# Kernel optimization log

Hardware: AMD Instinct MI355X
Metric: run time of the kernel (lower is better)

Reference implementation:

```python
import jax, jax.numpy as jnp
import numpy as np

B, TX, TS = 64, 2048, 10
D, L, NMELS, MAXR, R = 256, 1024, 80, 20, 2


def gru_cell(x, h, wih, whh, bih, bhh):
    # torch GRUCell: gates ordered (r, z, n)
    gi = x @ wih.T + bih
    gh = h @ whh.T + bhh
    ir, iz, inn = jnp.split(gi, 3, axis=-1)
    hr, hz, hn = jnp.split(gh, 3, axis=-1)
    r = jax.nn.sigmoid(ir + hr)
    z = jax.nn.sigmoid(iz + hz)
    n = jnp.tanh(inn + r * hn)
    return (1.0 - z) * n + z * h


def lstm_cell(x, h, c, wih, whh, bih, bhh):
    # torch LSTMCell: gates ordered (i, f, g, o)
    g = x @ wih.T + bih + h @ whh.T + bhh
    i, f, gg, o = jnp.split(g, 4, axis=-1)
    c_new = jax.nn.sigmoid(f) * c + jax.nn.sigmoid(i) * jnp.tanh(gg)
    h_new = jax.nn.sigmoid(o) * jnp.tanh(c_new)
    return h_new, c_new


def attention(enc, query, W, v):
    # u = v @ tanh(enc + W q); softmax over time
    qp = query @ W.T                                  # [B, D]
    u = jnp.tanh(enc + qp[:, None, :]) @ v            # [B, T]
    scores = jax.nn.softmax(u, axis=-1)               # [B, T]
    ctx = jnp.einsum('bt,btd->bd', scores, enc)       # [B, D]
    return scores, ctx


def setup_inputs() -> dict:
    key = jax.random.key(0)
    ks = jax.random.split(key, 40)
    n = lambda i, shape, s=0.02: jax.random.normal(ks[i], shape, dtype=jnp.float32) * s
    return {
        'encoder_seq': n(0, (B, TX, D), 1.0),
        'style_embed': n(1, (B, TS, D), 1.0),
        'prenet_in': n(2, (B, NMELS), 1.0),
        'h_text': n(3, (B, D), 1.0), 'h_style': n(4, (B, D), 1.0), 'h_attn': n(5, (B, D), 1.0),
        'h_r1': n(6, (B, L), 1.0), 'h_r2': n(7, (B, L), 1.0),
        'c_r1': n(8, (B, L), 1.0), 'c_r2': n(9, (B, L), 1.0),
        'cv_text': n(10, (B, D), 1.0), 'cv_style': n(11, (B, D), 1.0), 'cv': n(12, (B, D), 1.0),
        'fc1_w': n(13, (256, NMELS)), 'fc1_b': jnp.zeros((256,), jnp.float32),
        'fc2_w': n(14, (128, 256)), 'fc2_b': jnp.zeros((128,), jnp.float32),
        'tW': n(15, (D, D)), 'tv': n(16, (D,)),
        'sW': n(17, (D, D)), 'sv': n(18, (D,)),
        't_wih': n(19, (3 * D, D + 128)), 't_whh': n(20, (3 * D, D)),
        't_bih': jnp.zeros((3 * D,), jnp.float32), 't_bhh': jnp.zeros((3 * D,), jnp.float32),
        's_wih': n(21, (3 * D, D + 128)), 's_whh': n(22, (3 * D, D)),
        's_bih': jnp.zeros((3 * D,), jnp.float32), 's_bhh': jnp.zeros((3 * D,), jnp.float32),
        'a_wih': n(23, (3 * D, D + 128)), 'a_whh': n(24, (3 * D, D)),
        'a_bih': jnp.zeros((3 * D,), jnp.float32), 'a_bhh': jnp.zeros((3 * D,), jnp.float32),
        'ri_w': n(25, (L, 2 * D)), 'ri_b': jnp.zeros((L,), jnp.float32),
        'l1_wih': n(26, (4 * L, L)), 'l1_whh': n(27, (4 * L, L)),
        'l1_bih': jnp.zeros((4 * L,), jnp.float32), 'l1_bhh': jnp.zeros((4 * L,), jnp.float32),
        'l2_wih': n(28, (4 * L, L)), 'l2_whh': n(29, (4 * L, L)),
        'l2_bih': jnp.zeros((4 * L,), jnp.float32), 'l2_bhh': jnp.zeros((4 * L,), jnp.float32),
        'mp_w': n(30, (NMELS * MAXR, L)),
        't': 0,
    }


def reference(encoder_seq, style_embed, prenet_in, h_text, h_style, h_attn,
              h_r1, h_r2, c_r1, c_r2, cv_text, cv_style, cv,
              fc1_w, fc1_b, fc2_w, fc2_b, tW, tv, sW, sv,
              t_wih, t_whh, t_bih, t_bhh, s_wih, s_whh, s_bih, s_bhh,
              a_wih, a_whh, a_bih, a_bhh, ri_w, ri_b,
              l1_wih, l1_whh, l1_bih, l1_bhh, l2_wih, l2_whh, l2_bih, l2_bhh,
              mp_w, t):
    # PreNet (eval mode: no dropout)
    p = jax.nn.relu(prenet_in @ fc1_w.T + fc1_b)
    p = jax.nn.relu(p @ fc2_w.T + fc2_b)                      # [B, 128]

    text_in = jnp.concatenate([cv_text, p], axis=-1)          # [B, D+128]
    style_in = jnp.concatenate([cv_style, p], axis=-1)
    attn_in = jnp.concatenate([cv, p], axis=-1)

    h_text = gru_cell(text_in, h_text, t_wih, t_whh, t_bih, t_bhh)
    text_scores, cv_text = attention(encoder_seq, h_text, tW, tv)

    h_style = gru_cell(style_in, h_style, s_wih, s_whh, s_bih, s_bhh)
    style_scores, cv_style = attention(style_embed, h_style, sW, sv)

    cv_new = cv_text                                          # context_vec = text_context_vec
    h_attn = gru_cell(attn_in, h_attn, a_wih, a_whh, a_bih, a_bhh)

    x = jnp.concatenate([cv_new, h_attn], axis=1) @ ri_w.T + ri_b  # [B, L]
    h_r1, c_r1 = lstm_cell(x, h_r1, c_r1, l1_wih, l1_whh, l1_bih, l1_bhh)
    x = x + h_r1
    h_r2, c_r2 = lstm_cell(x, h_r2, c_r2, l2_wih, l2_whh, l2_bih, l2_bhh)
    x = x + h_r2

    mels = (x @ mp_w.T).reshape(B, NMELS, MAXR)[:, :, :R]     # [B, n_mels, r]
    return mels
```

## Files before the change

### kernel.cpp

```cpp
#include <hip/hip_runtime.h>
#include <hip/hip_bf16.h>

typedef unsigned short u16;
typedef unsigned int   u32;
typedef __attribute__((ext_vector_type(8))) short bf16x8;
typedef __attribute__((ext_vector_type(4))) float f32x4;

#define NB   64
#define NTX  2048
#define ND   256
#define NL   1024

#if __has_builtin(__builtin_amdgcn_exp2f)
#define EXP2F(x) __builtin_amdgcn_exp2f(x)
#else
#define EXP2F(x) exp2f(x)
#endif

__device__ __forceinline__ float rcp_fast(float x){
  float r;
  asm volatile("v_rcp_f32 %0, %1" : "=v"(r) : "v"(x));
  return r;
}

__device__ __forceinline__ u16 f2bf(float f){
  union { float f; u32 u; } c; c.f = f;
  return (u16)((c.u + 0x7fffu + ((c.u >> 16) & 1u)) >> 16);
}
__device__ __forceinline__ u32 pk2(float a, float b){
  return (u32)f2bf(a) | ((u32)f2bf(b) << 16);
}
__device__ __forceinline__ float sigmf(float x){ return 1.f/(1.f+__expf(-x)); }
__device__ __forceinline__ float tanhf_fast(float x){
  x = fminf(fmaxf(x, -15.f), 15.f);
  float e = __expf(2.f*x);
  return (e - 1.f) / (e + 1.f);
}
__device__ __forceinline__ float tanh_pade(float x){
  x = fminf(fmaxf(x, -4.f), 4.f);
  float t = x*x;
  float n = ((t + 378.f)*t + 17325.f)*t + 135135.f;
  float d = ((28.f*t + 3150.f)*t + 62370.f)*t + 135135.f;
  return x * n * rcp_fast(d);
}
__device__ __forceinline__ float dot_rowf(const float* __restrict__ row,
                                          const float* __restrict__ x, int K4){
  float acc = 0.f;
  for (int j = 0; j < K4; ++j){
    float4 w = *(const float4*)(row + j*4);
    const float* xp = x + j*4;
    acc += w.x*xp[0] + w.y*xp[1] + w.z*xp[2] + w.w*xp[3];
  }
  return acc;
}

__global__ __launch_bounds__(256) void k_pre1(
    const float* __restrict__ cv_text, const float* __restrict__ cv,
    const float* __restrict__ h_text,  const float* __restrict__ h_attn,
    const float* __restrict__ prenet_in,
    const float* __restrict__ fc1_w, const float* __restrict__ fc1_b,
    const float* __restrict__ h_r1, const float* __restrict__ h_r2,
    float* __restrict__ xtext, float* __restrict__ xattn,
    float* __restrict__ htT,  float* __restrict__ haT,
    float* __restrict__ p1T,
    u16* __restrict__ hb1, u16* __restrict__ hb2)
{
  __shared__ float ld[64][65];
  const int blk = blockIdx.x, tid = threadIdx.x;
  if (blk < 16){
    int a = blk >> 2; int c0 = (blk & 3)*64;
    const float* src = (a==0)?cv_text:(a==1)?cv:(a==2)?h_text:h_attn;
    float* dst = (a==0)?xtext:(a==1)?xattn:(a==2)?htT:haT;
    const int r = tid >> 2, q = tid & 3;
    #pragma unroll
    for (int i = 0; i < 4; ++i){
      float4 v = *(const float4*)(src + (size_t)r*256 + c0 + q*16 + i*4);
      ld[r][q*16+i*4+0] = v.x; ld[r][q*16+i*4+1] = v.y;
      ld[r][q*16+i*4+2] = v.z; ld[r][q*16+i*4+3] = v.w;
    }
    __syncthreads();
    const int cc = tid >> 2;
    #pragma unroll
    for (int i = 0; i < 4; ++i){
      int b0 = q*16 + i*4;
      float4 o = { ld[b0+0][cc], ld[b0+1][cc], ld[b0+2][cc], ld[b0+3][cc] };
      *(float4*)(dst + (size_t)(c0+cc)*64 + b0) = o;
    }
  } else if (blk < 80){
    const int wave = tid >> 6, lane = tid & 63;
    const int n = (blk - 16)*4 + wave;
    float acc = fc1_b[n];
    const float* wr = fc1_w + (size_t)n*80;
    const float* xr = prenet_in + (size_t)lane*80;
    #pragma unroll
    for (int k = 0; k < 80; k += 4){
      float4 w = *(const float4*)(wr + k);
      acc += w.x*xr[k] + w.y*xr[k+1] + w.z*xr[k+2] + w.w*xr[k+3];
    }
    p1T[n*64 + lane] = fmaxf(acc, 0.f);
  } else {
    const int t2 = blk - 80;
    const float* src = (t2 < 32) ? h_r1 : h_r2;
    u16* dst = (t2 < 32) ? hb1 : hb2;
    const int base = (t2 & 31)*2048 + tid*8;
    float4 a = *(const float4*)(src + base);
    float4 b = *(const float4*)(src + base + 4);
    uint4 o = { pk2(a.x,a.y), pk2(a.z,a.w), pk2(b.x,b.y), pk2(b.z,b.w) };
    *(uint4*)(dst + base) = o;
  }
}

__global__ __launch_bounds__(256) void k_pre2(
    const float* __restrict__ p1T,
    const float* __restrict__ fc2_w, const float* __restrict__ fc2_b,
    float* __restrict__ xtext, float* __restrict__ xattn)
{
  const int tid = threadIdx.x, w = tid >> 6, lane = tid & 63;
  const int n = blockIdx.x;
  __shared__ float red[4][64];
  float acc = 0.f;
  const float* wr = fc2_w + (size_t)n*256 + w*64;
  const float* xb = p1T + w*64*64 + lane;
  #pragma unroll
  for (int k = 0; k < 64; k += 4){
    float4 wv = *(const float4*)(wr + k);
    acc += wv.x*xb[(k+0)*64] + wv.y*xb[(k+1)*64]
         + wv.z*xb[(k+2)*64] + wv.w*xb[(k+3)*64];
  }
  red[w][lane] = acc;
  __syncthreads();
  if (w == 0){
    float v = fmaxf(red[0][lane]+red[1][lane]+red[2][lane]+red[3][lane] + fc2_b[n], 0.f);
    xtext[(size_t)(256+n)*64 + lane] = v;
    xattn[(size_t)(256+n)*64 + lane] = v;
  }
}

__global__ __launch_bounds__(512) void k_gru(
    const float* __restrict__ t_wih, const float* __restrict__ t_whh,
    const float* __restrict__ t_bih, const float* __restrict__ t_bhh,
    const float* __restrict__ a_wih, const float* __restrict__ a_whh,
    const float* __restrict__ a_bih, const float* __restrict__ a_bhh,
    const float* __restrict__ xtext, const float* __restrict__ xattn,
    const float* __restrict__ htT,  const float* __restrict__ haT,
    float* __restrict__ htnT, u16* __restrict__ xrib)
{
  const int tid = threadIdx.x, w = tid >> 6, lane = tid & 63;
  const int isA = blockIdx.x >= 256;
  const int d = blockIdx.x & 255;
  const float* wih = isA ? a_wih : t_wih;
  const float* whh = isA ? a_whh : t_whh;
  const float* xT  = isA ? xattn : xtext;
  const float* hT  = isA ? haT   : htT;
  __shared__ float red[8][6][64];
  float s0=0.f,s1=0.f,s2=0.f,s3=0.f,s4=0.f,s5=0.f;
  {
    const float* wr = wih + (size_t)d*384       + w*48;
    const float* wz = wih + (size_t)(256+d)*384 + w*48;
    const float* wn = wih + (size_t)(512+d)*384 + w*48;
    const float* xb = xT + w*48*64 + lane;
    #pragma unroll 4
    for (int k = 0; k < 48; k += 4){
      float4 ar = *(const float4*)(wr + k);
      float4 az = *(const float4*)(wz + k);
      float4 an = *(const float4*)(wn + k);
      float x0 = xb[(k+0)*64], x1 = xb[(k+1)*64];
      float x2 = xb[(k+2)*64], x3 = xb[(k+3)*64];
      s0 += ar.x*x0 + ar.y*x1 + ar.z*x2 + ar.w*x3;
      s1 += az.x*x0 + az.y*x1 + az.z*x2 + az.w*x3;
      s2 += an.x*x0 + an.y*x1 + an.z*x2 + an.w*x3;
    }
  }
  {
    const float* vr = whh + (size_t)d*256       + w*32;
    const float* vz = whh + (size_t)(256+d)*256 + w*32;
    const float* vn = whh + (size_t)(512+d)*256 + w*32;
    const float* hb = hT + w*32*64 + lane;
    #pragma unroll 4
    for (int k = 0; k < 32; k += 4){
      float4 ar = *(const float4*)(vr + k);
      float4 az = *(const float4*)(vz + k);
      float4 an = *(const float4*)(vn + k);
      float h0 = hb[(k+0)*64], h1 = hb[(k+1)*64];
      float h2 = hb[(k+2)*64], h3 = hb[(k+3)*64];
      s3 += ar.x*h0 + ar.y*h1 + ar.z*h2 + ar.w*h3;
      s4 += az.x*h0 + az.y*h1 + az.z*h2 + az.w*h3;
      s5 += an.x*h0 + an.y*h1 + an.z*h2 + an.w*h3;
    }
  }
  red[w][0][lane]=s0; red[w][1][lane]=s1; red[w][2][lane]=s2;
  red[w][3][lane]=s3; red[w][4][lane]=s4; red[w][5][lane]=s5;
  __syncthreads();
  if (w == 0){
    const float* bih = isA ? a_bih : t_bih;
    const float* bhh = isA ? a_bhh : t_bhh;
    float g6[6];
    #pragma unroll
    for (int i = 0; i < 6; ++i){
      float a = 0.f;
      #pragma unroll
      for (int ww = 0; ww < 8; ++ww) a += red[ww][i][lane];
      g6[i] = a;
    }
    float gir = bih[d]     + g6[0];
    float giz = bih[256+d] + g6[1];
    float gin = bih[512+d] + g6[2];
    float ghr = bhh[d]     + g6[3];
    float ghz = bhh[256+d] + g6[4];
    float ghn = bhh[512+d] + g6[5];
    float hd = hT[d*64 + lane];
    float r  = sigmf(gir + ghr), z = sigmf(giz + ghz);
    float nn = tanhf_fast(gin + r*ghn);
    float hnew = (1.f - z)*nn + z*hd;
    if (isA) xrib[(size_t)lane*512 + 256 + d] = f2bf(hnew);
    else     htnT[(size_t)d*64 + lane]        = hnew;
  }
}

__global__ __launch_bounds__(256) void k_qp(
    const float* __restrict__ tWm, const float* __restrict__ htnT,
    float* __restrict__ qp)
{
  const int tid = threadIdx.x, w = tid >> 6, lane = tid & 63;
  const int d = blockIdx.x;
  __shared__ float red[4][64];
  float acc = 0.f;
  const float* wr = tWm + (size_t)d*256 + w*64;
  const float* xb = htnT + w*64*64 + lane;
  #pragma unroll
  for (int k = 0; k < 64; k += 4){
    float4 wv = *(const float4*)(wr + k);
    acc += wv.x*xb[(k+0)*64] + wv.y*xb[(k+1)*64]
         + wv.z*xb[(k+2)*64] + wv.w*xb[(k+3)*64];
  }
  red[w][lane] = acc;
  __syncthreads();
  if (w == 0)
    qp[lane*ND + d] = red[0][lane]+red[1][lane]+red[2][lane]+red[3][lane];
}

__global__ __launch_bounds__(256) void k_attn_part(
    const float* __restrict__ enc, const float* __restrict__ qp,
    const float* __restrict__ tv,  float* __restrict__ attnP)
{
  const int tid = threadIdx.x, b = blockIdx.x, ch = blockIdx.y;
  const int w = tid >> 6, lane = tid & 63;
  const float L2E = 1.4426950408f;
  __shared__ float qpL[256], vL[256];
  __shared__ float part[4][16][65];
  __shared__ float wbc[4][16];
  __shared__ float ctxL[4][256], sL[4];
  qpL[tid] = qp[b*ND + tid];
  vL[tid]  = tv[tid];
  __syncthreads();

  const float q0 = qpL[lane*4+0], q1 = qpL[lane*4+1], q2 = qpL[lane*4+2], q3 = qpL[lane*4+3];
  const float v0 = vL[lane*4+0],  v1 = vL[lane*4+1],  v2 = vL[lane*4+2],  v3 = vL[lane*4+3];

  const float* base = enc + ((size_t)b*NTX + (size_t)ch*64 + w*16)*ND + lane*4;
  float4 ev[16];
  #pragma unroll
  for (int i = 0; i < 16; ++i) ev[i] = *(const float4*)(base + (size_t)i*ND);

  #pragma unroll
  for (int i = 0; i < 16; ++i){
    float t0 = tanh_pade(ev[i].x + q0);
    float t1 = tanh_pade(ev[i].y + q1);
    float t2 = tanh_pade(ev[i].z + q2);
    float t3 = tanh_pade(ev[i].w + q3);
    part[w][i][lane] = v0*t0 + v1*t1 + v2*t2 + v3*t3;
  }
  __syncthreads();

  {
    const int rr = lane >> 2, q4 = lane & 3;
    float s = 0.f;
    #pragma unroll
    for (int i = 0; i < 16; ++i) s += part[w][rr][q4*16 + i];
    s += __shfl_xor(s, 1);
    s += __shfl_xor(s, 2);
    if (q4 == 0) wbc[w][rr] = EXP2F(s * L2E);
  }
  __syncthreads();

  float cx0=0.f, cx1=0.f, cx2=0.f, cx3=0.f, sacc=0.f;
  #pragma unroll
  for (int r = 0; r < 16; ++r){
    float wv = wbc[w][r];
    sacc += wv;
    cx0 = __builtin_fmaf(wv, ev[r].x, cx0);
    cx1 = __builtin_fmaf(wv, ev[r].y, cx1);
    cx2 = __builtin_fmaf(wv, ev[r].z, cx2);
    cx3 = __builtin_fmaf(wv, ev[r].w, cx3);
  }
  ctxL[w][lane*4+0]=cx0; ctxL[w][lane*4+1]=cx1;
  ctxL[w][lane*4+2]=cx2; ctxL[w][lane*4+3]=cx3;
  if (lane == 0) sL[w] = sacc;
  __syncthreads();
  float c = ctxL[0][tid]+ctxL[1][tid]+ctxL[2][tid]+ctxL[3][tid];
  float* dst = attnP + ((size_t)b*32 + ch)*257;
  dst[tid] = c;
  if (tid == 0) dst[256] = sL[0]+sL[1]+sL[2]+sL[3];
}

__global__ __launch_bounds__(256) void k_attn_red(
    const float* __restrict__ attnP, u16* __restrict__ xrib)
{
  const int tid = threadIdx.x, b = blockIdx.x;
  float c = 0.f, s = 0.f;
  for (int ch = 0; ch < 32; ++ch){
    const float* src = attnP + ((size_t)b*32 + ch)*257;
    c += src[tid]; s += src[256];
  }
  xrib[(size_t)b*512 + tid] = f2bf(c / s);
}


__global__ __launch_bounds__(512) void k_mm_ri(
    const u16* __restrict__ xrib, const float* __restrict__ ri_w,
    const float* __restrict__ ri_b, float* __restrict__ x0,
    u16* __restrict__ x0b)
{
  __shared__ float Rs[8][4][4][65];
  const int tid = threadIdx.x, lane = tid & 63, w = tid >> 6;
  const int n0 = blockIdx.x * 16;
  f32x4 acc[4];
  #pragma unroll
  for (int i = 0; i < 4; ++i) acc[i] = (f32x4){0.f,0.f,0.f,0.f};
  const int kbase = w*64;
  const float* wr = ri_w + (size_t)(n0 + (lane & 15))*512 + kbase + (lane >> 4)*8;
  const u16* xs = xrib + (size_t)(lane & 15)*512 + kbase + (lane >> 4)*8;
  #pragma unroll
  for (int t = 0; t < 2; ++t){
    float4 wa = *(const float4*)(wr + t*32);
    float4 wb = *(const float4*)(wr + t*32 + 4);
    union { bf16x8 v; uint4 u; } bf;
    bf.u.x = pk2(wa.x,wa.y); bf.u.y = pk2(wa.z,wa.w);
    bf.u.z = pk2(wb.x,wb.y); bf.u.w = pk2(wb.z,wb.w);
    #pragma unroll
    for (int fb = 0; fb < 4; ++fb){
      union { bf16x8 v; uint4 u; } af;
      af.u = *(const uint4*)(xs + fb*16*512 + t*32);
      acc[fb] = __builtin_amdgcn_mfma_f32_16x16x32_bf16(af.v, bf.v, acc[fb], 0, 0, 0);
    }
  }
  #pragma unroll
  for (int fb = 0; fb < 4; ++fb)
    #pragma unroll
    for (int r = 0; r < 4; ++r) Rs[w][fb][r][lane] = acc[fb][r];
  __syncthreads();
  if (tid < 256){
    const int b = tid >> 2, c4 = (tid & 3)*4;
    const int fb = b >> 4, q = (b >> 2) & 3, reg = b & 3;
    #pragma unroll
    for (int cc = 0; cc < 4; ++cc){
      const int c = c4 + cc;
      float v = ri_b[n0 + c];
      #pragma unroll
      for (int ww = 0; ww < 8; ++ww) v += Rs[ww][fb][reg][q*16 + c];
      x0[(size_t)b*1024 + n0 + c]  = v;
      x0b[(size_t)b*1024 + n0 + c] = f2bf(v);
    }
  }
}

__global__ __launch_bounds__(1024) void k_lstm(
    const float* __restrict__ Wih, const float* __restrict__ Whh,
    const u16* __restrict__ xb, const u16* __restrict__ hb,
    const float* __restrict__ bih, const float* __restrict__ bhh,
    const float* __restrict__ c_in,
    const float* __restrict__ xin, float* __restrict__ xout,
    u16* __restrict__ xoutb)
{
  __shared__ float Rs[16][4][4][65];
  const int tid = threadIdx.x, lane = tid & 63, w = tid >> 6;
  const int j0 = blockIdx.x * 4;
  const float* W = (w < 8) ? Wih : Whh;
  const u16*   X = (w < 8) ? xb  : hb;
  const int kbase = (w & 7) * 128;

  f32x4 acc[4];
  #pragma unroll
  for (int i = 0; i < 4; ++i) acc[i] = (f32x4){0.f,0.f,0.f,0.f};
  const int r16 = lane & 15;
  const int g = r16 >> 2, jq = r16 & 3;
  const float* wr = W + (size_t)(g*1024 + j0 + jq)*1024 + kbase + (lane >> 4)*8;
  #pragma unroll
  for (int t = 0; t < 4; ++t){
    float4 wa = *(const float4*)(wr + t*32);
    float4 wb = *(const float4*)(wr + t*32 + 4);
    union { bf16x8 v; uint4 u; } bf;
    bf.u.x = pk2(wa.x,wa.y); bf.u.y = pk2(wa.z,wa.w);
    bf.u.z = pk2(wb.x,wb.y); bf.u.w = pk2(wb.z,wb.w);
    #pragma unroll
    for (int fb = 0; fb < 4; ++fb){
      union { bf16x8 v; uint4 u; } af;
      af.u = *(const uint4*)(X + (size_t)(fb*16 + r16)*1024 + kbase + (lane >> 4)*8 + t*32);
      acc[fb] = __builtin_amdgcn_mfma_f32_16x16x32_bf16(af.v, bf.v, acc[fb], 0, 0, 0);
    }
  }
  #pragma unroll
  for (int fb = 0; fb < 4; ++fb)
    #pragma unroll
    for (int r = 0; r < 4; ++r) Rs[w][fb][r][lane] = acc[fb][r];
  __syncthreads();

  if (tid < 256){
    const int b  = tid >> 2, jq2 = tid & 3;
    const int j  = j0 + jq2;
    const int fb = b >> 4, q = (b >> 2) & 3, reg = b & 3;
    float gate[4];
    #pragma unroll
    for (int gg = 0; gg < 4; ++gg){
      const int li = q*16 + gg*4 + jq2;
      float a = bih[gg*1024 + j] + bhh[gg*1024 + j];
      #pragma unroll
      for (int ww = 0; ww < 16; ++ww) a += Rs[ww][fb][reg][li];
      gate[gg] = a;
    }
    float ii = sigmf(gate[0]), ff = sigmf(gate[1]);
    float gv = tanhf_fast(gate[2]), oo = sigmf(gate[3]);
    float cc = ff * c_in[(size_t)b*1024 + j] + ii * gv;
    float hh = oo * tanhf_fast(cc);
    float xo = xin[(size_t)b*1024 + j] + hh;
    xout[(size_t)b*1024 + j]  = xo;
    xoutb[(size_t)b*1024 + j] = f2bf(xo);
  }
}

__global__ __launch_bounds__(256) void k_mels(
    const float* __restrict__ x2, const float* __restrict__ mp_w,
    float* __restrict__ out)
{
  const int tid = threadIdx.x, b = blockIdx.x;
  __shared__ float xL[NL];
  #pragma unroll
  for (int i = 0; i < 4; ++i){
    int j = tid + 256*i;
    xL[j] = x2[(size_t)b*NL + j];
  }
  __syncthreads();
  if (tid < 160){
    int m = tid >> 1, r = tid & 1;
    float acc = dot_rowf(mp_w + (size_t)(m*20 + r)*NL, xL, 256);
    out[b*160 + tid] = acc;
  }
}

extern "C" void kernel_launch(void* const* d_in, const int* in_sizes, int n_in,
                              void* d_out, int out_size, void* d_ws, size_t ws_size,
                              hipStream_t stream)
{
  (void)in_sizes; (void)n_in; (void)out_size; (void)ws_size;
  const float* enc     = (const float*)d_in[0];
  const float* pre_in  = (const float*)d_in[2];
  const float* h_text  = (const float*)d_in[3];
  const float* h_attn  = (const float*)d_in[5];
  const float* h_r1    = (const float*)d_in[6];
  const float* h_r2    = (const float*)d_in[7];
  const float* c_r1    = (const float*)d_in[8];
  const float* c_r2    = (const float*)d_in[9];
  const float* cv_text = (const float*)d_in[10];
  const float* cv      = (const float*)d_in[12];
  const float* fc1_w   = (const float*)d_in[13];
  const float* fc1_b   = (const float*)d_in[14];
  const float* fc2_w   = (const float*)d_in[15];
  const float* fc2_b   = (const float*)d_in[16];
  const float* tWm     = (const float*)d_in[17];
  const float* tv      = (const float*)d_in[18];
  const float* t_wih   = (const float*)d_in[21];
  const float* t_whh   = (const float*)d_in[22];
  const float* t_bih   = (const float*)d_in[23];
  const float* t_bhh   = (const float*)d_in[24];
  const float* a_wih   = (const float*)d_in[29];
  const float* a_whh   = (const float*)d_in[30];
  const float* a_bih   = (const float*)d_in[31];
  const float* a_bhh   = (const float*)d_in[32];
  const float* ri_w    = (const float*)d_in[33];
  const float* ri_b    = (const float*)d_in[34];
  const float* l1_wih  = (const float*)d_in[35];
  const float* l1_whh  = (const float*)d_in[36];
  const float* l1_bih  = (const float*)d_in[37];
  const float* l1_bhh  = (const float*)d_in[38];
  const float* l2_wih  = (const float*)d_in[39];
  const float* l2_whh  = (const float*)d_in[40];
  const float* l2_bih  = (const float*)d_in[41];
  const float* l2_bhh  = (const float*)d_in[42];
  const float* mp_w    = (const float*)d_in[43];

  float* ws    = (float*)d_ws;
  float* qp    = ws;
  float* attnP = qp    + 16384;
  float* x0    = attnP + 526336;
  float* x1    = x0    + 65536;
  float* x2    = x1    + 65536;
  float* xtext = x2    + 65536;
  float* xattn = xtext + 24576;
  float* htT   = xattn + 24576;
  float* haT   = htT   + 16384;
  float* htnT  = haT   + 16384;
  float* p1T   = htnT  + 16384;
  u16*   hb1   = (u16*)(p1T + 16384);
  u16*   hb2   = hb1 + 65536;
  u16*   xrib  = hb2 + 65536;
  u16*   x0b   = xrib + 32768;
  u16*   x1b   = x0b + 65536;
  u16*   x2b   = x1b + 65536;

  k_pre1<<<144, 256, 0, stream>>>(cv_text, cv, h_text, h_attn,
      pre_in, fc1_w, fc1_b, h_r1, h_r2,
      xtext, xattn, htT, haT, p1T, hb1, hb2);
  k_pre2<<<128, 256, 0, stream>>>(p1T, fc2_w, fc2_b, xtext, xattn);
  k_gru<<<512, 512, 0, stream>>>(t_wih, t_whh, t_bih, t_bhh,
      a_wih, a_whh, a_bih, a_bhh, xtext, xattn, htT, haT, htnT, xrib);
  k_qp<<<256, 256, 0, stream>>>(tWm, htnT, qp);

  k_attn_part<<<dim3(64,32), 256, 0, stream>>>(enc, qp, tv, attnP);
  k_attn_red<<<64, 256, 0, stream>>>(attnP, xrib);

  k_mm_ri<<<64, 512, 0, stream>>>(xrib, ri_w, ri_b, x0, x0b);

  k_lstm<<<256, 1024, 0, stream>>>(l1_wih, l1_whh, x0b, hb1,
      l1_bih, l1_bhh, c_r1, x0, x1, x1b);
  k_lstm<<<256, 1024, 0, stream>>>(l2_wih, l2_whh, x1b, hb2,
      l2_bih, l2_bhh, c_r2, x1, x2, x2b);

  k_mels<<<64, 256, 0, stream>>>(x2, mp_w, (float*)d_out);
}
```

Baseline: 111.6 us.

## Restructure attention partial kernel into per-wave streaming with double-buffered loads

The attention partial kernel drops shared memory and block barriers. Each wave now computes its row scores with a full-wave shuffle reduction, applies the exponent, and accumulates context itself. It processes 32 rows in double-buffered groups of 8 register loads so memory fetches overlap compute. The grid is halved and each wave writes its own partial, which doubles the partial buffer and the reduction loop length. Costs are 64 partials per batch in the reduction and six serial shuffles per row.

New measurement: 140.6 us. 1.26x slower.

```diff
diff --git a/kernel.cpp b/kernel.cpp
--- a/kernel.cpp
+++ b/kernel.cpp
@@ -239,6 +239,27 @@
     qp[lane*ND + d] = red[0][lane]+red[1][lane]+red[2][lane]+red[3][lane];
 }
 
+#define ATTN_PROC(E) \
+  { \
+    _Pragma("unroll") \
+    for (int i = 0; i < 8; ++i){ \
+      float t0 = tanh_pade(E[i].x + qv.x); \
+      float t1 = tanh_pade(E[i].y + qv.y); \
+      float t2 = tanh_pade(E[i].z + qv.z); \
+      float t3 = tanh_pade(E[i].w + qv.w); \
+      float s = vv.x*t0 + vv.y*t1 + vv.z*t2 + vv.w*t3; \
+      s += __shfl_xor(s, 1);  s += __shfl_xor(s, 2); \
+      s += __shfl_xor(s, 4);  s += __shfl_xor(s, 8); \
+      s += __shfl_xor(s, 16); s += __shfl_xor(s, 32); \
+      float wv_ = EXP2F(s * L2E); \
+      sacc += wv_; \
+      cx0 = __builtin_fmaf(wv_, E[i].x, cx0); \
+      cx1 = __builtin_fmaf(wv_, E[i].y, cx1); \
+      cx2 = __builtin_fmaf(wv_, E[i].z, cx2); \
+      cx3 = __builtin_fmaf(wv_, E[i].w, cx3); \
+    } \
+  }
+
 __global__ __launch_bounds__(256) void k_attn_part(
     const float* __restrict__ enc, const float* __restrict__ qp,
     const float* __restrict__ tv,  float* __restrict__ attnP)
@@ -246,61 +267,30 @@
   const int tid = threadIdx.x, b = blockIdx.x, ch = blockIdx.y;
   const int w = tid >> 6, lane = tid & 63;
   const float L2E = 1.4426950408f;
-  __shared__ float qpL[256], vL[256];
-  __shared__ float part[4][16][65];
-  __shared__ float wbc[4][16];
-  __shared__ float ctxL[4][256], sL[4];
-  qpL[tid] = qp[b*ND + tid];
-  vL[tid]  = tv[tid];
-  __syncthreads();
-
-  const float q0 = qpL[lane*4+0], q1 = qpL[lane*4+1], q2 = qpL[lane*4+2], q3 = qpL[lane*4+3];
-  const float v0 = vL[lane*4+0],  v1 = vL[lane*4+1],  v2 = vL[lane*4+2],  v3 = vL[lane*4+3];
-
-  const float* base = enc + ((size_t)b*NTX + (size_t)ch*64 + w*16)*ND + lane*4;
-  float4 ev[16];
-  #pragma unroll
-  for (int i = 0; i < 16; ++i) ev[i] = *(const float4*)(base + (size_t)i*ND);
-
-  #pragma unroll
-  for (int i = 0; i < 16; ++i){
-    float t0 = tanh_pade(ev[i].x + q0);
-    float t1 = tanh_pade(ev[i].y + q1);
-    float t2 = tanh_pade(ev[i].z + q2);
-    float t3 = tanh_pade(ev[i].w + q3);
-    part[w][i][lane] = v0*t0 + v1*t1 + v2*t2 + v3*t3;
-  }
-  __syncthreads();
-
-  {
-    const int rr = lane >> 2, q4 = lane & 3;
-    float s = 0.f;
-    #pragma unroll
-    for (int i = 0; i < 16; ++i) s += part[w][rr][q4*16 + i];
-    s += __shfl_xor(s, 1);
-    s += __shfl_xor(s, 2);
-    if (q4 == 0) wbc[w][rr] = EXP2F(s * L2E);
-  }
-  __syncthreads();
+  const float4 qv = *(const float4*)(qp + b*ND + lane*4);
+  const float4 vv = *(const float4*)(tv + lane*4);
+  const float* base = enc + ((size_t)b*NTX + (size_t)ch*128 + w*32)*ND + lane*4;
 
   float cx0=0.f, cx1=0.f, cx2=0.f, cx3=0.f, sacc=0.f;
-  #pragma unroll
-  for (int r = 0; r < 16; ++r){
-    float wv = wbc[w][r];
-    sacc += wv;
-    cx0 = __builtin_fmaf(wv, ev[r].x, cx0);
-    cx1 = __builtin_fmaf(wv, ev[r].y, cx1);
-    cx2 = __builtin_fmaf(wv, ev[r].z, cx2);
-    cx3 = __builtin_fmaf(wv, ev[r].w, cx3);
-  }
-  ctxL[w][lane*4+0]=cx0; ctxL[w][lane*4+1]=cx1;
-  ctxL[w][lane*4+2]=cx2; ctxL[w][lane*4+3]=cx3;
-  if (lane == 0) sL[w] = sacc;
-  __syncthreads();
-  float c = ctxL[0][tid]+ctxL[1][tid]+ctxL[2][tid]+ctxL[3][tid];
-  float* dst = attnP + ((size_t)b*32 + ch)*257;
-  dst[tid] = c;
-  if (tid == 0) dst[256] = sL[0]+sL[1]+sL[2]+sL[3];
+  float4 evA[8], evB[8];
+
+  #pragma unroll
+  for (int i = 0; i < 8; ++i) evA[i] = *(const float4*)(base + (size_t)i*ND);
+  #pragma unroll
+  for (int i = 0; i < 8; ++i) evB[i] = *(const float4*)(base + (size_t)(8+i)*ND);
+  ATTN_PROC(evA)
+  #pragma unroll
+  for (int i = 0; i < 8; ++i) evA[i] = *(const float4*)(base + (size_t)(16+i)*ND);
+  ATTN_PROC(evB)
+  #pragma unroll
+  for (int i = 0; i < 8; ++i) evB[i] = *(const float4*)(base + (size_t)(24+i)*ND);
+  ATTN_PROC(evA)
+  ATTN_PROC(evB)
+
+  float* dst = attnP + ((size_t)(b*64 + ch*4 + w))*257;
+  float4 o = {cx0, cx1, cx2, cx3};
+  *(float4*)(dst + lane*4) = o;
+  if (lane == 0) dst[256] = sacc;
 }
 
 __global__ __launch_bounds__(256) void k_attn_red(
@@ -308,8 +298,8 @@
 {
   const int tid = threadIdx.x, b = blockIdx.x;
   float c = 0.f, s = 0.f;
-  for (int ch = 0; ch < 32; ++ch){
-    const float* src = attnP + ((size_t)b*32 + ch)*257;
+  for (int p = 0; p < 64; ++p){
+    const float* src = attnP + ((size_t)(b*64 + p))*257;
     c += src[tid]; s += src[256];
   }
   xrib[(size_t)b*512 + tid] = f2bf(c / s);
@@ -491,7 +481,7 @@
   float* ws    = (float*)d_ws;
   float* qp    = ws;
   float* attnP = qp    + 16384;
-  float* x0    = attnP + 526336;
+  float* x0    = attnP + 1052672;
   float* x1    = x0    + 65536;
   float* x2    = x1    + 65536;
   float* xtext = x2    + 65536;
@@ -515,7 +505,7 @@
       a_wih, a_whh, a_bih, a_bhh, xtext, xattn, htT, haT, htnT, xrib);
   k_qp<<<256, 256, 0, stream>>>(tWm, htnT, qp);
 
-  k_attn_part<<<dim3(64,32), 256, 0, stream>>>(enc, qp, tv, attnP);
+  k_attn_part<<<dim3(64,16), 256, 0, stream>>>(enc, qp, tv, attnP);
   k_attn_red<<<64, 256, 0, stream>>>(attnP, xrib);
 
   k_mm_ri<<<64, 512, 0, stream>>>(xrib, ri_w, ri_b, x0, x0b);
```
